# Optimization experiments

Hardware: AMD Instinct MI355X
Metric: run time of the kernel (lower is better)

## Reference

```python
import jax, jax.numpy as jnp
import numpy as np

N_NODES = 50000
N_EDGES = 640000
D = 128


def gcn_conv(x, W, b, row, col, n):
    """PyG GCNConv: linear -> add self-loops -> symmetric norm -> scatter-add -> bias."""
    x = x @ W.T                                   # [N, D]
    sl = jnp.arange(n, dtype=row.dtype)
    row_sl = jnp.concatenate([row, sl])           # source nodes (messages from x_j)
    col_sl = jnp.concatenate([col, sl])           # target nodes (aggregation index)
    ones = jnp.ones(row_sl.shape[0], dtype=x.dtype)
    deg = jax.ops.segment_sum(ones, col_sl, num_segments=n)
    dinv = jnp.where(deg > 0, 1.0 / jnp.sqrt(deg), 0.0)
    norm = dinv[row_sl] * dinv[col_sl]            # [E+N]
    msgs = x[row_sl] * norm[:, None]              # [E+N, D] gather+scale
    out = jax.ops.segment_sum(msgs, col_sl, num_segments=n)
    return out + b


def setup_inputs() -> dict:
    key = jax.random.key(0)
    ks = jax.random.split(key, 12)
    s = 1.0 / np.sqrt(D)
    inp = {
        "z": jax.random.normal(ks[0], (N_NODES, D), dtype=jnp.float32),
        "edge_index": jax.random.randint(ks[1], (2, N_EDGES), 0, N_NODES, dtype=jnp.int64),
        "t": jax.random.randint(ks[2], (N_NODES,), 0, 1000, dtype=jnp.int32),
        "Wt1": jax.random.uniform(ks[3], (D, 1), jnp.float32, -1.0, 1.0),
        "bt1": jax.random.uniform(ks[4], (D,), jnp.float32, -1.0, 1.0),
        "Wt2": jax.random.uniform(ks[5], (D, D), jnp.float32, -s, s),
        "bt2": jax.random.uniform(ks[6], (D,), jnp.float32, -s, s),
        "W1": jax.random.uniform(ks[7], (D, D), jnp.float32, -s, s),
        "b1": jnp.zeros((D,), jnp.float32),
        "W2": jax.random.uniform(ks[8], (D, D), jnp.float32, -s, s),
        "b2": jnp.zeros((D,), jnp.float32),
    }
    return inp


def reference(z, edge_index, t, Wt1, bt1, Wt2, bt2, W1, b1, W2, b2):
    n = z.shape[0]
    row, col = edge_index[0], edge_index[1]
    # time MLP: Linear(1,D) -> GELU (exact) -> Linear(D,D)
    tf = t.astype(z.dtype)[:, None]               # [N, 1]
    t_emb = jax.nn.gelu(tf @ Wt1.T + bt1, approximate=False) @ Wt2.T + bt2
    h1 = jax.nn.elu(gcn_conv(z, W1, b1, row, col, n) + t_emb)
    noise_pred = gcn_conv(h1, W2, b2, row, col, n)
    return noise_pred
```

## Files before the change

kernel.cpp:

```cpp
#include <hip/hip_runtime.h>
#include <hip/hip_bf16.h>
#include <math.h>

#define D 128
#define ELLW 64
#define NB 256
#define CHUNK 8192
#define NTAB 16
#define GEMM1_ROWS 256

typedef __attribute__((ext_vector_type(8))) short short8v;
typedef __attribute__((ext_vector_type(4))) float f32x4;

__device__ __forceinline__ float gelu_exact(float x) {
    return 0.5f * x * (1.0f + erff(x * 0.70710678118654752440f));
}
__device__ __forceinline__ float elu1(float x) {
    return x > 0.f ? x : expm1f(x);
}
__device__ __forceinline__ unsigned short f2bf(float f) {
    unsigned int u = __float_as_uint(f);
    u += 0x7fffu + ((u >> 16) & 1u);
    return (unsigned short)(u >> 16);
}
__device__ __forceinline__ float bflo(unsigned int u) {
    return __uint_as_float(u << 16);
}
__device__ __forceinline__ float bfhi(unsigned int u) {
    return __uint_as_float(u & 0xffff0000u);
}

__global__ __launch_bounds__(256) void bin_prep_kernel(
    const int* __restrict__ ep,
    unsigned int* __restrict__ binsrc, int* __restrict__ segstart,
    const float* __restrict__ Wt2, float* __restrict__ WT,
    const float* __restrict__ wt1, const float* __restrict__ bt1,
    float* __restrict__ G,
    const float* __restrict__ W1, unsigned short* __restrict__ W1h,
    const float* __restrict__ W2, unsigned short* __restrict__ W2h,
    int E, int part, int nchunk, int nt) {
    const int tid = threadIdx.x;
    const int bid = blockIdx.x;

    if (bid >= nchunk) {
        int idx = (bid - nchunk) * 256 + tid;
        if (idx < 16384) {
            int j = idx >> 7, k = idx & 127;
            WT[k * 128 + j] = Wt2[idx];
            return;
        }
        idx -= 16384;
        if (idx < nt * D) {
            int v = idx >> 7, k = idx & 127;
            G[idx] = gelu_exact(fmaf((float)v, wt1[k], bt1[k]));
            return;
        }
        idx -= nt * D;
        if (idx < 16384) { W1h[idx] = f2bf(W1[idx]); return; }
        idx -= 16384;
        if (idx < 16384) { W2h[idx] = f2bf(W2[idx]); }
        return;
    }

    __shared__ int anyS;
    __shared__ int hist[NB];
    __shared__ int curx[NB];
    __shared__ int offs[NB];
    __shared__ int wtot[4];
    __shared__ unsigned int buf[CHUNK];
    if (tid == 0) anyS = 0;
    __syncthreads();
    for (int i = tid; i < 2000; i += 256)
        if (ep[2 * i + 1] != 0) anyS = 1;
    hist[tid] = 0;
    __syncthreads();
    const int mode = anyS ? 0 : 1;
    const int e0 = bid * CHUNK;
    const int e1 = min(e0 + CHUNK, E);

    for (int e = e0 + tid; e < e1; e += 256) {
        int c = mode ? ep[2 * (E + e)] : ep[E + e];
        atomicAdd(&hist[c / part], 1);
    }
    __syncthreads();
    int v = hist[tid];
    int lane = tid & 63, wv = tid >> 6;
    int s = v;
    #pragma unroll
    for (int off = 1; off < 64; off <<= 1) {
        int t = __shfl_up(s, off);
        if (lane >= off) s += t;
    }
    if (lane == 63) wtot[wv] = s;
    __syncthreads();
    if (tid == 0) {
        int run = 0;
        #pragma unroll
        for (int w = 0; w < 4; ++w) { int tm = wtot[w]; wtot[w] = run; run += tm; }
    }
    __syncthreads();
    int excl = wtot[wv] + s - v;
    offs[tid] = excl;
    curx[tid] = excl;
    __syncthreads();
    for (int e = e0 + tid; e < e1; e += 256) {
        int r = mode ? ep[2 * e] : ep[e];
        int c = mode ? ep[2 * (E + e)] : ep[E + e];
        int p = atomicAdd(&curx[c / part], 1);
        buf[p] = ((unsigned)c << 16) | (unsigned)r;
    }
    __syncthreads();
    const int cnt = e1 - e0;
    for (int i = tid; i < cnt; i += 256) binsrc[(size_t)e0 + i] = buf[i];
    segstart[bid * (NB + 1) + tid] = offs[tid];
    if (tid == 0) segstart[bid * (NB + 1) + NB] = cnt;
}

__global__ __launch_bounds__(512) void k2_fused_kernel(
    const unsigned int* __restrict__ binsrc, const int* __restrict__ segstart,
    int* __restrict__ deg, float* __restrict__ dinv, unsigned short* __restrict__ ell,
    const float* __restrict__ G, const float* __restrict__ WTt2,
    const float* __restrict__ bias, const float* __restrict__ bias2,
    float* __restrict__ table,
    const float* __restrict__ z, const unsigned short* __restrict__ W1h,
    unsigned short* __restrict__ xwh,
    int nchunk, int part, int n, int nt) {
    __shared__ __align__(16) char smem[8 * 32 * 136 * 2];
    const int tid = threadIdx.x;
    const int bid = blockIdx.x;

    if (bid < NB) {
        int* cnt = (int*)smem;
        int* s0s = cnt + 256;
        int* s1s = s0s + 128;
        const int lane = tid & 63, wv = tid >> 6;
        const int lo = bid * part;
        const int hi = min(lo + part, n);
        if (tid < part) cnt[tid] = 0;
        for (int i = tid; i < nchunk; i += 512) {
            s0s[i] = segstart[i * (NB + 1) + bid];
            s1s[i] = segstart[i * (NB + 1) + bid + 1];
        }
        __syncthreads();
        for (int ch = wv; ch < nchunk; ch += 8) {
            int s0 = s0s[ch], s1 = s1s[ch];
            const unsigned int* p = binsrc + (size_t)ch * CHUNK;
            for (int i = s0 + lane; i < s1; i += 64) {
                unsigned int ec = p[i];
                int c = (int)(ec >> 16);
                int rank = atomicAdd(&cnt[c - lo], 1);
                if (rank < ELLW) ell[(size_t)c * ELLW + rank] = (unsigned short)(ec & 0xffffu);
            }
        }
        __syncthreads();
        for (int i = tid; lo + i < hi; i += 512) {
            int dv = cnt[i];
            deg[lo + i] = dv;
            dinv[lo + i] = rsqrtf((float)(dv + 1));
        }
        return;
    }

    if (bid < NB + NTAB) {
        float (*Wsh)[68] = (float(*)[68])smem;
        const int tb = bid - NB;
        const int r0 = (tb >> 1) * 128;
        const int jb = (tb & 1) * 64;
        #pragma unroll
        for (int rep = 0; rep < 4; ++rep) {
            int flat = rep * 512 + tid;
            int k = flat >> 4;
            int jj = (flat & 15) * 4;
            *(float4*)&Wsh[k][jj] = *(const float4*)(WTt2 + k * D + jb + jj);
        }
        __syncthreads();
        if (tid < 256) {
            const int tx = tid & 7, ty = tid >> 3;
            const int rbase = r0 + ty * 4;
            const int jcol = tx * 8;
            float acc[4][8];
            #pragma unroll
            for (int i = 0; i < 4; ++i)
                #pragma unroll
                for (int j = 0; j < 8; ++j) acc[i][j] = 0.f;
            #pragma unroll 2
            for (int k0 = 0; k0 < 128; k0 += 4) {
                float4 a[4];
                #pragma unroll
                for (int i = 0; i < 4; ++i) {
                    int rr = rbase + i;
                    a[i] = (rr < nt) ? *(const float4*)(G + (size_t)rr * D + k0)
                                     : make_float4(0.f, 0.f, 0.f, 0.f);
                }
                float4 wv[4][2];
                #pragma unroll
                for (int kk = 0; kk < 4; ++kk) {
                    wv[kk][0] = *(const float4*)&Wsh[k0 + kk][jcol];
                    wv[kk][1] = *(const float4*)&Wsh[k0 + kk][jcol + 4];
                }
                #pragma unroll
                for (int i = 0; i < 4; ++i) {
                    float av[4] = {a[i].x, a[i].y, a[i].z, a[i].w};
                    #pragma unroll
                    for (int kk = 0; kk < 4; ++kk) {
                        acc[i][0] = fmaf(av[kk], wv[kk][0].x, acc[i][0]);
                        acc[i][1] = fmaf(av[kk], wv[kk][0].y, acc[i][1]);
                        acc[i][2] = fmaf(av[kk], wv[kk][0].z, acc[i][2]);
                        acc[i][3] = fmaf(av[kk], wv[kk][0].w, acc[i][3]);
                        acc[i][4] = fmaf(av[kk], wv[kk][1].x, acc[i][4]);
                        acc[i][5] = fmaf(av[kk], wv[kk][1].y, acc[i][5]);
                        acc[i][6] = fmaf(av[kk], wv[kk][1].z, acc[i][6]);
                        acc[i][7] = fmaf(av[kk], wv[kk][1].w, acc[i][7]);
                    }
                }
            }
            float4 ba = *(const float4*)(bias + jb + jcol);
            float4 bb = *(const float4*)(bias2 + jb + jcol);
            float4 b0 = make_float4(ba.x + bb.x, ba.y + bb.y, ba.z + bb.z, ba.w + bb.w);
            ba = *(const float4*)(bias + jb + jcol + 4);
            bb = *(const float4*)(bias2 + jb + jcol + 4);
            float4 b1v = make_float4(ba.x + bb.x, ba.y + bb.y, ba.z + bb.z, ba.w + bb.w);
            #pragma unroll
            for (int i = 0; i < 4; ++i) {
                int rr = rbase + i;
                if (rr < nt) {
                    float4 o0, o1;
                    o0.x = acc[i][0] + b0.x; o0.y = acc[i][1] + b0.y;
                    o0.z = acc[i][2] + b0.z; o0.w = acc[i][3] + b0.w;
                    o1.x = acc[i][4] + b1v.x; o1.y = acc[i][5] + b1v.y;
                    o1.z = acc[i][6] + b1v.z; o1.w = acc[i][7] + b1v.w;
                    *(float4*)(table + (size_t)rr * D + jb + jcol) = o0;
                    *(float4*)(table + (size_t)rr * D + jb + jcol + 4) = o1;
                }
            }
        }
        return;
    }

    {
        const int gb = bid - NB - NTAB;
        const int w   = tid >> 6;
        const int l   = tid & 63;
        const int l15 = l & 15;
        const int l4  = l >> 4;
        const int rb  = gb * GEMM1_ROWS + w * 32;

        f32x4 acc[8][2];
        #pragma unroll
        for (int jt = 0; jt < 8; ++jt)
            #pragma unroll
            for (int rt = 0; rt < 2; ++rt)
                acc[jt][rt] = (f32x4){0.f, 0.f, 0.f, 0.f};

        #pragma unroll
        for (int ks = 0; ks < 4; ++ks) {
            const int kk = ks * 32 + l4 * 8;
            short8v bfrag[2];
            #pragma unroll
            for (int rt = 0; rt < 2; ++rt) {
                int r = rb + rt * 16 + l15;
                const float* af = z + (size_t)r * D + kk;
                float4 x0, x1;
                if (r < n) { x0 = *(const float4*)af; x1 = *(const float4*)(af + 4); }
                else       { x0 = make_float4(0,0,0,0); x1 = x0; }
                union { short8v v; unsigned short u[8]; } cv;
                cv.u[0] = f2bf(x0.x); cv.u[1] = f2bf(x0.y);
                cv.u[2] = f2bf(x0.z); cv.u[3] = f2bf(x0.w);
                cv.u[4] = f2bf(x1.x); cv.u[5] = f2bf(x1.y);
                cv.u[6] = f2bf(x1.z); cv.u[7] = f2bf(x1.w);
                bfrag[rt] = cv.v;
            }
            #pragma unroll
            for (int jt = 0; jt < 8; ++jt) {
                short8v afrag = *(const short8v*)(W1h + (size_t)(jt * 16 + l15) * D + kk);
                acc[jt][0] = __builtin_amdgcn_mfma_f32_16x16x32_bf16(afrag, bfrag[0], acc[jt][0], 0, 0, 0);
                acc[jt][1] = __builtin_amdgcn_mfma_f32_16x16x32_bf16(afrag, bfrag[1], acc[jt][1], 0, 0, 0);
            }
        }

        unsigned short* eb = (unsigned short*)smem + w * (32 * 136);
        #pragma unroll
        for (int jt = 0; jt < 8; ++jt) {
            #pragma unroll
            for (int rt = 0; rt < 2; ++rt) {
                int lr = rt * 16 + l15;
                f32x4 a = acc[jt][rt];
                unsigned int p0 = (unsigned int)f2bf(a[0]) | ((unsigned int)f2bf(a[1]) << 16);
                unsigned int p1 = (unsigned int)f2bf(a[2]) | ((unsigned int)f2bf(a[3]) << 16);
                int col = jt * 16 + l4 * 4;
                *(unsigned int*)(eb + lr * 136 + col)     = p0;
                *(unsigned int*)(eb + lr * 136 + col + 2) = p1;
            }
        }
        __syncthreads();
        #pragma unroll
        for (int rep = 0; rep < 8; ++rep) {
            int lr = rep * 4 + l4;
            int c8 = l15 * 8;
            int row = rb + lr;
            if (row < n)
                *(uint4*)(xwh + (size_t)row * D + c8) = *(const uint4*)(eb + lr * 136 + c8);
        }
    }
}

__global__ __launch_bounds__(256) void gemm_mfma(
    const unsigned short* __restrict__ Ain,
    const unsigned short* __restrict__ Wh,
    const float* __restrict__ dinv,
    unsigned short* __restrict__ outh,
    int n) {
    __shared__ unsigned short eb_all[4][32][136];
    const int tid = threadIdx.x;
    const int w   = tid >> 6;
    const int l   = tid & 63;
    const int l15 = l & 15;
    const int l4  = l >> 4;

    const int rb = blockIdx.x * 128 + w * 32;

    f32x4 acc[8][2];
    #pragma unroll
    for (int jt = 0; jt < 8; ++jt)
        #pragma unroll
        for (int rt = 0; rt < 2; ++rt)
            acc[jt][rt] = (f32x4){0.f, 0.f, 0.f, 0.f};

    #pragma unroll
    for (int ks = 0; ks < 4; ++ks) {
        const int kk = ks * 32 + l4 * 8;
        short8v bfrag[2];
        #pragma unroll
        for (int rt = 0; rt < 2; ++rt) {
            int r = rb + rt * 16 + l15;
            if (r < n) bfrag[rt] = *(const short8v*)(Ain + (size_t)r * D + kk);
            else {
                union { short8v v; unsigned short u[8]; } z0;
                #pragma unroll
                for (int q = 0; q < 8; ++q) z0.u[q] = 0;
                bfrag[rt] = z0.v;
            }
        }
        #pragma unroll
        for (int jt = 0; jt < 8; ++jt) {
            short8v afrag = *(const short8v*)(Wh + (size_t)(jt * 16 + l15) * D + kk);
            acc[jt][0] = __builtin_amdgcn_mfma_f32_16x16x32_bf16(afrag, bfrag[0], acc[jt][0], 0, 0, 0);
            acc[jt][1] = __builtin_amdgcn_mfma_f32_16x16x32_bf16(afrag, bfrag[1], acc[jt][1], 0, 0, 0);
        }
    }

    int r0i = rb + l15, r1i = rb + 16 + l15;
    float dv0 = (r0i < n) ? dinv[r0i] : 0.f;
    float dv1 = (r1i < n) ? dinv[r1i] : 0.f;

    unsigned short* eb = &eb_all[w][0][0];
    #pragma unroll
    for (int jt = 0; jt < 8; ++jt) {
        #pragma unroll
        for (int rt = 0; rt < 2; ++rt) {
            int lr = rt * 16 + l15;
            float s = rt ? dv1 : dv0;
            f32x4 a = acc[jt][rt];
            unsigned int p0 = (unsigned int)f2bf(a[0] * s) | ((unsigned int)f2bf(a[1] * s) << 16);
            unsigned int p1 = (unsigned int)f2bf(a[2] * s) | ((unsigned int)f2bf(a[3] * s) << 16);
            int col = jt * 16 + l4 * 4;
            *(unsigned int*)(eb + lr * 136 + col)     = p0;
            *(unsigned int*)(eb + lr * 136 + col + 2) = p1;
        }
    }
    __syncthreads();
    #pragma unroll
    for (int rep = 0; rep < 8; ++rep) {
        int lr = rep * 4 + l4;
        int c8 = l15 * 8;
        int row = rb + lr;
        if (row < n)
            *(uint4*)(outh + (size_t)row * D + c8) = *(const uint4*)(eb + lr * 136 + c8);
    }
}

template <int EPI, int PRESC>
__global__ __launch_bounds__(256) void gather_bf16(
    const unsigned short* __restrict__ xh, const int* __restrict__ deg,
    const float* __restrict__ dinv,
    const unsigned short* __restrict__ ell,
    const float* __restrict__ table, const int* __restrict__ tvec,
    const float* __restrict__ bias,
    void* __restrict__ dst, int n) {
    int wid = (blockIdx.x * 256 + threadIdx.x) >> 6;
    if (wid >= n) return;
    int lane = threadIdx.x & 63;
    const int lo = lane * 2;

    int dgr = deg[wid];
    float di = dinv[wid];
    int dg = dgr > ELLW ? ELLW : dgr;
    const unsigned short* row = ell + (size_t)wid * ELLW;

    float2 ep;
    if (EPI == 0) {
        ep = *(const float2*)(bias + lo);
    } else {
        int tv = tvec[wid];
        ep = *(const float2*)(table + (size_t)tv * D + lo);
    }

    unsigned int sv = *(const unsigned int*)(xh + (size_t)wid * D + lo);
    float sx, sy;
    if (PRESC) { sx = bflo(sv);      sy = bfhi(sv); }
    else       { sx = di * bflo(sv); sy = di * bfhi(sv); }

    int e = 0;
    for (; e + 8 < dg; e += 16) {
        uint4 pk0 = *(const uint4*)(row + e);
        uint4 pk1 = *(const uint4*)(row + e + 8);
        int id[16];
        id[0]=(int)(pk0.x&0xffffu); id[1]=(int)(pk0.x>>16);
        id[2]=(int)(pk0.y&0xffffu); id[3]=(int)(pk0.y>>16);
        id[4]=(int)(pk0.z&0xffffu); id[5]=(int)(pk0.z>>16);
        id[6]=(int)(pk0.w&0xffffu); id[7]=(int)(pk0.w>>16);
        id[8]=(int)(pk1.x&0xffffu); id[9]=(int)(pk1.x>>16);
        id[10]=(int)(pk1.y&0xffffu); id[11]=(int)(pk1.y>>16);
        id[12]=(int)(pk1.z&0xffffu); id[13]=(int)(pk1.z>>16);
        id[14]=(int)(pk1.w&0xffffu); id[15]=(int)(pk1.w>>16);
        unsigned int u[16];
        float wgt[16];
        #pragma unroll
        for (int j = 0; j < 16; ++j) {
            int rc = id[j] < n ? id[j] : 0;
            if (!PRESC) wgt[j] = dinv[rc];
            u[j] = *(const unsigned int*)(xh + (size_t)rc * D + lo);
        }
        #pragma unroll
        for (int j = 0; j < 16; ++j) {
            bool vld = (e + j) < dg;
            if (PRESC) {
                sx += vld ? bflo(u[j]) : 0.f;
                sy += vld ? bfhi(u[j]) : 0.f;
            } else {
                float m = vld ? wgt[j] : 0.f;
                sx = fmaf(m, bflo(u[j]), sx);
                sy = fmaf(m, bfhi(u[j]), sy);
            }
        }
    }
    if (e < dg) {
        uint4 pk = *(const uint4*)(row + e);
        int id[8];
        id[0]=(int)(pk.x&0xffffu); id[1]=(int)(pk.x>>16);
        id[2]=(int)(pk.y&0xffffu); id[3]=(int)(pk.y>>16);
        id[4]=(int)(pk.z&0xffffu); id[5]=(int)(pk.z>>16);
        id[6]=(int)(pk.w&0xffffu); id[7]=(int)(pk.w>>16);
        unsigned int u[8];
        float wgt[8];
        #pragma unroll
        for (int j = 0; j < 8; ++j) {
            int rc = id[j] < n ? id[j] : 0;
            if (!PRESC) wgt[j] = dinv[rc];
            u[j] = *(const unsigned int*)(xh + (size_t)rc * D + lo);
        }
        #pragma unroll
        for (int j = 0; j < 8; ++j) {
            bool vld = (e + j) < dg;
            if (PRESC) {
                sx += vld ? bflo(u[j]) : 0.f;
                sy += vld ? bfhi(u[j]) : 0.f;
            } else {
                float m = vld ? wgt[j] : 0.f;
                sx = fmaf(m, bflo(u[j]), sx);
                sy = fmaf(m, bfhi(u[j]), sy);
            }
        }
    }

    float ox = di * sx + ep.x;
    float oy = di * sy + ep.y;
    if (EPI == 0) {
        *(float2*)((float*)dst + (size_t)wid * D + lo) = make_float2(ox, oy);
    } else {
        ox = elu1(ox); oy = elu1(oy);
        unsigned int p = (unsigned int)f2bf(ox) | ((unsigned int)f2bf(oy) << 16);
        *(unsigned int*)((unsigned short*)dst + (size_t)wid * D + lo) = p;
    }
}

extern "C" void kernel_launch(void* const* d_in, const int* in_sizes, int n_in,
                              void* d_out, int out_size, void* d_ws, size_t ws_size,
                              hipStream_t stream) {
    const float* z   = (const float*)d_in[0];
    const int*   ep  = (const int*)d_in[1];
    const int*   t   = (const int*)d_in[2];
    const float* Wt1 = (const float*)d_in[3];
    const float* bt1 = (const float*)d_in[4];
    const float* Wt2 = (const float*)d_in[5];
    const float* bt2 = (const float*)d_in[6];
    const float* W1  = (const float*)d_in[7];
    const float* b1  = (const float*)d_in[8];
    const float* W2  = (const float*)d_in[9];
    const float* b2  = (const float*)d_in[10];
    float* out = (float*)d_out;

    const int N = in_sizes[0] / D;
    const int E = in_sizes[1] / 2;
    const int NT = 1000;
    const int PART = (N + NB - 1) / NB;
    const int NCHUNK = (E + CHUNK - 1) / CHUNK;

    size_t off = 0;
    auto carve = [&](size_t nbytes) -> void* {
        void* p = (void*)((char*)d_ws + off);
        off += (nbytes + 255) & ~(size_t)255;
        return p;
    };
    int*            deg     = (int*)carve((size_t)N * 4);
    float*          dinv    = (float*)carve((size_t)N * 4);
    unsigned short* ell     = (unsigned short*)carve((size_t)N * ELLW * 2);
    unsigned int*   binsrc  = (unsigned int*)carve((size_t)NCHUNK * CHUNK * 4);
    int*            segstart= (int*)carve((size_t)NCHUNK * (NB + 1) * 4);
    float*          WTt2    = (float*)carve((size_t)16384 * 4);
    float*          G       = (float*)carve((size_t)NT * D * 4);
    float*          table   = (float*)carve((size_t)NT * D * 4);
    unsigned short* W1h     = (unsigned short*)carve((size_t)16384 * 2);
    unsigned short* W2h     = (unsigned short*)carve((size_t)16384 * 2);
    unsigned short* xwh     = (unsigned short*)carve((size_t)N * D * 2);
    unsigned short* acch    = (unsigned short*)carve((size_t)N * D * 2);
    (void)ws_size; (void)n_in; (void)out_size;

    int prep_elems = 16384 + NT * D + 16384 + 16384;
    int prep_blocks = (prep_elems + 255) / 256;
    bin_prep_kernel<<<NCHUNK + prep_blocks, 256, 0, stream>>>(
        ep, binsrc, segstart, Wt2, WTt2, Wt1, bt1, G, W1, W1h, W2, W2h,
        E, PART, NCHUNK, NT);

    int gemm1_blocks = (N + GEMM1_ROWS - 1) / GEMM1_ROWS;
    k2_fused_kernel<<<NB + NTAB + gemm1_blocks, 512, 0, stream>>>(
        binsrc, segstart, deg, dinv, ell, G, WTt2, bt2, b1, table,
        z, W1h, xwh, NCHUNK, PART, N, NT);

    gather_bf16<1, 0><<<(N * 64 + 255) / 256, 256, 0, stream>>>(
        xwh, deg, dinv, ell, table, t, nullptr, acch, N);

    gemm_mfma<<<(N + 127) / 128, 256, 0, stream>>>(acch, W2h, dinv, xwh, N);

    gather_bf16<0, 1><<<(N * 64 + 255) / 256, 256, 0, stream>>>(
        xwh, deg, dinv, ell, nullptr, nullptr, b2, out, N);
}
```

Measured before the change: 130.9 us.

## Fuse layer-1 gather with second GEMM through LDS staging

Each wave now gathers and normalizes 32 node rows (with the time-embedding epilogue and ELU), stores them as bf16 in LDS, then runs the MFMA GEMM with W2 directly from LDS. This removes the intermediate global buffer write/read and one kernel launch. Output goes to a separate buffer so other blocks can still read xwh. The cost is far fewer concurrent waves for the latency-bound gather, since each wave serially processes 32 nodes.

New measurement: 151.9 us. +16.1%, slower.

```diff
diff --git a/kernel.cpp b/kernel.cpp
--- a/kernel.cpp
+++ b/kernel.cpp
@@ -304,20 +304,90 @@
     }
 }
 
-__global__ __launch_bounds__(256) void gemm_mfma(
-    const unsigned short* __restrict__ Ain,
-    const unsigned short* __restrict__ Wh,
-    const float* __restrict__ dinv,
+__global__ __launch_bounds__(256) void gather_gemm_kernel(
+    const unsigned short* __restrict__ xh,
+    const int* __restrict__ deg, const float* __restrict__ dinv,
+    const unsigned short* __restrict__ ell,
+    const float* __restrict__ table, const int* __restrict__ tvec,
+    const unsigned short* __restrict__ W2h,
     unsigned short* __restrict__ outh,
     int n) {
-    __shared__ unsigned short eb_all[4][32][136];
+    __shared__ unsigned short lds[4][32][136];
     const int tid = threadIdx.x;
-    const int w   = tid >> 6;
-    const int l   = tid & 63;
-    const int l15 = l & 15;
-    const int l4  = l >> 4;
-
+    const int w = tid >> 6, l = tid & 63;
+    const int l15 = l & 15, l4 = l >> 4;
     const int rb = blockIdx.x * 128 + w * 32;
+    const int lo = l * 2;
+
+    for (int idx = 0; idx < 32; ++idx) {
+        int node = rb + idx;
+        unsigned int packed = 0;
+        if (node < n) {
+            int dgr = deg[node];
+            float di = dinv[node];
+            int dg = dgr > ELLW ? ELLW : dgr;
+            const unsigned short* row = ell + (size_t)node * ELLW;
+            int tv = tvec[node];
+            float2 epv = *(const float2*)(table + (size_t)tv * D + lo);
+            unsigned int sv = *(const unsigned int*)(xh + (size_t)node * D + lo);
+            float sx = di * bflo(sv), sy = di * bfhi(sv);
+            int e = 0;
+            for (; e + 8 < dg; e += 16) {
+                uint4 pk0 = *(const uint4*)(row + e);
+                uint4 pk1 = *(const uint4*)(row + e + 8);
+                int id[16];
+                id[0]=(int)(pk0.x&0xffffu); id[1]=(int)(pk0.x>>16);
+                id[2]=(int)(pk0.y&0xffffu); id[3]=(int)(pk0.y>>16);
+                id[4]=(int)(pk0.z&0xffffu); id[5]=(int)(pk0.z>>16);
+                id[6]=(int)(pk0.w&0xffffu); id[7]=(int)(pk0.w>>16);
+                id[8]=(int)(pk1.x&0xffffu); id[9]=(int)(pk1.x>>16);
+                id[10]=(int)(pk1.y&0xffffu); id[11]=(int)(pk1.y>>16);
+                id[12]=(int)(pk1.z&0xffffu); id[13]=(int)(pk1.z>>16);
+                id[14]=(int)(pk1.w&0xffffu); id[15]=(int)(pk1.w>>16);
+                unsigned int u[16];
+                float wgt[16];
+                #pragma unroll
+                for (int j = 0; j < 16; ++j) {
+                    int rc = id[j] < n ? id[j] : 0;
+                    wgt[j] = dinv[rc];
+                    u[j] = *(const unsigned int*)(xh + (size_t)rc * D + lo);
+                }
+                #pragma unroll
+                for (int j = 0; j < 16; ++j) {
+                    float m = (e + j) < dg ? wgt[j] : 0.f;
+                    sx = fmaf(m, bflo(u[j]), sx);
+                    sy = fmaf(m, bfhi(u[j]), sy);
+                }
+            }
+            if (e < dg) {
+                uint4 pk = *(const uint4*)(row + e);
+                int id[8];
+                id[0]=(int)(pk.x&0xffffu); id[1]=(int)(pk.x>>16);
+                id[2]=(int)(pk.y&0xffffu); id[3]=(int)(pk.y>>16);
+                id[4]=(int)(pk.z&0xffffu); id[5]=(int)(pk.z>>16);
+                id[6]=(int)(pk.w&0xffffu); id[7]=(int)(pk.w>>16);
+                unsigned int u[8];
+                float wgt[8];
+                #pragma unroll
+                for (int j = 0; j < 8; ++j) {
+                    int rc = id[j] < n ? id[j] : 0;
+                    wgt[j] = dinv[rc];
+                    u[j] = *(const unsigned int*)(xh + (size_t)rc * D + lo);
+                }
+                #pragma unroll
+                for (int j = 0; j < 8; ++j) {
+                    float m = (e + j) < dg ? wgt[j] : 0.f;
+                    sx = fmaf(m, bflo(u[j]), sx);
+                    sy = fmaf(m, bfhi(u[j]), sy);
+                }
+            }
+            float ox = elu1(di * sx + epv.x);
+            float oy = elu1(di * sy + epv.y);
+            packed = (unsigned int)f2bf(ox) | ((unsigned int)f2bf(oy) << 16);
+        }
+        *(unsigned int*)&lds[w][idx][lo] = packed;
+    }
+    __syncthreads();
 
     f32x4 acc[8][2];
     #pragma unroll
@@ -331,29 +401,22 @@
         const int kk = ks * 32 + l4 * 8;
         short8v bfrag[2];
         #pragma unroll
-        for (int rt = 0; rt < 2; ++rt) {
-            int r = rb + rt * 16 + l15;
-            if (r < n) bfrag[rt] = *(const short8v*)(Ain + (size_t)r * D + kk);
-            else {
-                union { short8v v; unsigned short u[8]; } z0;
-                #pragma unroll
-                for (int q = 0; q < 8; ++q) z0.u[q] = 0;
-                bfrag[rt] = z0.v;
-            }
-        }
+        for (int rt = 0; rt < 2; ++rt)
+            bfrag[rt] = *(const short8v*)&lds[w][rt * 16 + l15][kk];
         #pragma unroll
         for (int jt = 0; jt < 8; ++jt) {
-            short8v afrag = *(const short8v*)(Wh + (size_t)(jt * 16 + l15) * D + kk);
+            short8v afrag = *(const short8v*)(W2h + (size_t)(jt * 16 + l15) * D + kk);
             acc[jt][0] = __builtin_amdgcn_mfma_f32_16x16x32_bf16(afrag, bfrag[0], acc[jt][0], 0, 0, 0);
             acc[jt][1] = __builtin_amdgcn_mfma_f32_16x16x32_bf16(afrag, bfrag[1], acc[jt][1], 0, 0, 0);
         }
     }
+    __syncthreads();
 
     int r0i = rb + l15, r1i = rb + 16 + l15;
     float dv0 = (r0i < n) ? dinv[r0i] : 0.f;
     float dv1 = (r1i < n) ? dinv[r1i] : 0.f;
 
-    unsigned short* eb = &eb_all[w][0][0];
+    unsigned short* eb = &lds[w][0][0];
     #pragma unroll
     for (int jt = 0; jt < 8; ++jt) {
         #pragma unroll
@@ -379,14 +442,12 @@
     }
 }
 
-template <int EPI, int PRESC>
-__global__ __launch_bounds__(256) void gather_bf16(
+__global__ __launch_bounds__(256) void gather_out_kernel(
     const unsigned short* __restrict__ xh, const int* __restrict__ deg,
     const float* __restrict__ dinv,
     const unsigned short* __restrict__ ell,
-    const float* __restrict__ table, const int* __restrict__ tvec,
     const float* __restrict__ bias,
-    void* __restrict__ dst, int n) {
+    float* __restrict__ dst, int n) {
     int wid = (blockIdx.x * 256 + threadIdx.x) >> 6;
     if (wid >= n) return;
     int lane = threadIdx.x & 63;
@@ -397,18 +458,10 @@
     int dg = dgr > ELLW ? ELLW : dgr;
     const unsigned short* row = ell + (size_t)wid * ELLW;
 
-    float2 ep;
-    if (EPI == 0) {
-        ep = *(const float2*)(bias + lo);
-    } else {
-        int tv = tvec[wid];
-        ep = *(const float2*)(table + (size_t)tv * D + lo);
-    }
+    float2 ep = *(const float2*)(bias + lo);
 
     unsigned int sv = *(const unsigned int*)(xh + (size_t)wid * D + lo);
-    float sx, sy;
-    if (PRESC) { sx = bflo(sv);      sy = bfhi(sv); }
-    else       { sx = di * bflo(sv); sy = di * bfhi(sv); }
+    float sx = bflo(sv), sy = bfhi(sv);
 
     int e = 0;
     for (; e + 8 < dg; e += 16) {
@@ -424,24 +477,16 @@
         id[12]=(int)(pk1.z&0xffffu); id[13]=(int)(pk1.z>>16);
         id[14]=(int)(pk1.w&0xffffu); id[15]=(int)(pk1.w>>16);
         unsigned int u[16];
-        float wgt[16];
         #pragma unroll
         for (int j = 0; j < 16; ++j) {
             int rc = id[j] < n ? id[j] : 0;
-            if (!PRESC) wgt[j] = dinv[rc];
             u[j] = *(const unsigned int*)(xh + (size_t)rc * D + lo);
         }
         #pragma unroll
         for (int j = 0; j < 16; ++j) {
             bool vld = (e + j) < dg;
-            if (PRESC) {
-                sx += vld ? bflo(u[j]) : 0.f;
-                sy += vld ? bfhi(u[j]) : 0.f;
-            } else {
-                float m = vld ? wgt[j] : 0.f;
-                sx = fmaf(m, bflo(u[j]), sx);
-                sy = fmaf(m, bfhi(u[j]), sy);
-            }
+            sx += vld ? bflo(u[j]) : 0.f;
+            sy += vld ? bfhi(u[j]) : 0.f;
         }
     }
     if (e < dg) {
@@ -452,36 +497,20 @@
         id[4]=(int)(pk.z&0xffffu); id[5]=(int)(pk.z>>16);
         id[6]=(int)(pk.w&0xffffu); id[7]=(int)(pk.w>>16);
         unsigned int u[8];
-        float wgt[8];
         #pragma unroll
         for (int j = 0; j < 8; ++j) {
             int rc = id[j] < n ? id[j] : 0;
-            if (!PRESC) wgt[j] = dinv[rc];
             u[j] = *(const unsigned int*)(xh + (size_t)rc * D + lo);
         }
         #pragma unroll
         for (int j = 0; j < 8; ++j) {
             bool vld = (e + j) < dg;
-            if (PRESC) {
-                sx += vld ? bflo(u[j]) : 0.f;
-                sy += vld ? bfhi(u[j]) : 0.f;
-            } else {
-                float m = vld ? wgt[j] : 0.f;
-                sx = fmaf(m, bflo(u[j]), sx);
-                sy = fmaf(m, bfhi(u[j]), sy);
-            }
-        }
-    }
-
-    float ox = di * sx + ep.x;
-    float oy = di * sy + ep.y;
-    if (EPI == 0) {
-        *(float2*)((float*)dst + (size_t)wid * D + lo) = make_float2(ox, oy);
-    } else {
-        ox = elu1(ox); oy = elu1(oy);
-        unsigned int p = (unsigned int)f2bf(ox) | ((unsigned int)f2bf(oy) << 16);
-        *(unsigned int*)((unsigned short*)dst + (size_t)wid * D + lo) = p;
-    }
+            sx += vld ? bflo(u[j]) : 0.f;
+            sy += vld ? bfhi(u[j]) : 0.f;
+        }
+    }
+
+    *(float2*)(dst + (size_t)wid * D + lo) = make_float2(di * sx + ep.x, di * sy + ep.y);
 }
 
 extern "C" void kernel_launch(void* const* d_in, const int* in_sizes, int n_in,
@@ -523,7 +552,7 @@
     unsigned short* W1h     = (unsigned short*)carve((size_t)16384 * 2);
     unsigned short* W2h     = (unsigned short*)carve((size_t)16384 * 2);
     unsigned short* xwh     = (unsigned short*)carve((size_t)N * D * 2);
-    unsigned short* acch    = (unsigned short*)carve((size_t)N * D * 2);
+    unsigned short* xwh2    = (unsigned short*)carve((size_t)N * D * 2);
     (void)ws_size; (void)n_in; (void)out_size;
 
     int prep_elems = 16384 + NT * D + 16384 + 16384;
@@ -537,11 +566,9 @@
         binsrc, segstart, deg, dinv, ell, G, WTt2, bt2, b1, table,
         z, W1h, xwh, NCHUNK, PART, N, NT);
 
-    gather_bf16<1, 0><<<(N * 64 + 255) / 256, 256, 0, stream>>>(
-        xwh, deg, dinv, ell, table, t, nullptr, acch, N);
-
-    gemm_mfma<<<(N + 127) / 128, 256, 0, stream>>>(acch, W2h, dinv, xwh, N);
-
-    gather_bf16<0, 1><<<(N * 64 + 255) / 256, 256, 0, stream>>>(
-        xwh, deg, dinv, ell, nullptr, nullptr, b2, out, N);
-}
+    gather_gemm_kernel<<<(N + 127) / 128, 256, 0, stream>>>(
+        xwh, deg, dinv, ell, table, t, W2h, xwh2, N);
+
+    gather_out_kernel<<<(N * 64 + 255) / 256, 256, 0, stream>>>(
+        xwh2, deg, dinv, ell, b2, out, N);
+}
```
